# Kernel tuning notes

Hardware: AMD Instinct MI355X
Metric: run time of the kernel (lower is better)

The kernel has to match this reference:

```python
import jax, jax.numpy as jnp
import numpy as np

N, E, C, NEF, OUT, NUM_ANGLE = 20000, 160000, 32, 1, 128, 7
F = 2 * C + NEF  # edge_fdim = 65


def setup_inputs() -> dict:
    rng = np.random.default_rng(0)
    row = rng.integers(0, N, size=E).astype(np.int32)
    col = rng.integers(0, N, size=E).astype(np.int32)
    # Line-graph incidence pairs (a, b): edge a = (i,j) feeds edge b = (j,k), i.e. col[a] == row[b].
    sort_idx = np.argsort(row, kind='stable')
    row_sorted = row[sort_idx]
    starts = np.searchsorted(row_sorted, col, 'left')
    ends = np.searchsorted(row_sorted, col, 'right')
    counts = ends - starts
    total = int(counts.sum())
    line_src = np.repeat(np.arange(E, dtype=np.int32), counts)
    base = np.repeat(starts, counts)
    within = np.arange(total, dtype=np.int64) - np.repeat(np.cumsum(counts) - counts, counts)
    line_dst = sort_idx[base + within].astype(np.int32)

    key = jax.random.key(0)
    k = jax.random.split(key, 5)
    return {
        'x': jax.random.normal(k[0], (N, C), jnp.float32),
        'edge_attr': jax.random.normal(k[1], (E, NEF), jnp.float32),
        'pos': jax.random.normal(k[2], (N, 3), jnp.float32),
        'W_msg': jax.random.normal(k[3], (OUT, NUM_ANGLE * 2 * F), jnp.float32) * 0.02,
        'b_msg': jax.random.normal(k[4], (OUT,), jnp.float32) * 0.01,
        'edge_index': jnp.asarray(np.stack([row, col]), jnp.int32),
        'line_src': jnp.asarray(line_src),
        'line_dst': jnp.asarray(line_dst),
    }


def reference(x, edge_attr, pos, W_msg, b_msg, edge_index, line_src, line_dst):
    row, col = edge_index[0], edge_index[1]
    num_node = x.shape[0]
    num_edge = row.shape[0]

    # edge_f = [x_row | x_col | edge_attr]  -> [E, F]
    edge_f = jnp.concatenate([x[row], x[col], edge_attr], axis=1)

    # Line graph: edge a=(i,j) feeds edge b=(j,k). Angle at shared node j.
    j = col[line_src]
    u = pos[row[line_src]] - pos[j]  # j -> i
    v = pos[col[line_dst]] - pos[j]  # j -> k
    cos = jnp.sum(u * v, axis=-1) / (
        jnp.linalg.norm(u, axis=-1) * jnp.linalg.norm(v, axis=-1) + 1e-8)
    ang = jnp.arccos(jnp.clip(cos, -1.0 + 1e-7, 1.0 - 1e-7))  # [0, pi]
    abin = jnp.clip((ang / jnp.pi * NUM_ANGLE).astype(jnp.int32), 0, NUM_ANGLE - 1)

    # Per target edge, accumulate neighbor-edge features into (angle bin, in/out slot).
    seg_in = line_dst.astype(jnp.int32) * (NUM_ANGLE * 2) + abin * 2      # incoming a -> b
    seg_out = line_src.astype(jnp.int32) * (NUM_ANGLE * 2) + abin * 2 + 1  # outgoing b seen from a
    vals = jnp.concatenate([edge_f[line_src], edge_f[line_dst]], axis=0)  # [2L, F]
    segs = jnp.concatenate([seg_in, seg_out], axis=0)
    msg = jax.ops.segment_sum(vals, segs, num_segments=num_edge * NUM_ANGLE * 2)
    msg = msg.reshape(num_edge, NUM_ANGLE * 2 * F)  # [E, 910]

    # output = self.message(message)  (Linear with bias)
    edge_hidden = msg @ W_msg.T + b_msg  # [E, OUT]

    # scatter_add into destination nodes (edge_index[1])
    update = jax.ops.segment_sum(edge_hidden, col, num_segments=num_node)  # [N, OUT]
    return update
```

## Files before the change

### kernel.cpp

```cpp
#include <hip/hip_runtime.h>
#include <stdint.h>

#define N_NODES 20000
#define E_EDGES 160000
#define C_DIM 32
#define OUT_DIM 128
#define K_REAL 910
#define KPH 480
#define DEG_CAP 64
#define SEG 1024
#define NSEG 20
#define MT_A (E_EDGES/256)
#define NROWS_B 20224
#define MT_B (NROWS_B/256)

typedef __attribute__((ext_vector_type(4))) float f32x4;
typedef __attribute__((ext_vector_type(8))) short short8;

__device__ __forceinline__ float bf2f(unsigned short u){
  union { unsigned int i; float f; } v; v.i = ((unsigned int)u) << 16; return v.f;
}
__device__ __forceinline__ unsigned short f2bf(float f){
  union { float f; unsigned int i; } v; v.f = f;
  unsigned int i = v.i;
  unsigned int r = (i + 0x7FFFu + ((i >> 16) & 1u)) >> 16;
  return (unsigned short)r;
}
__device__ __forceinline__ float ldv(const void* p, size_t i, int isbf){
  return isbf ? bf2f(((const unsigned short*)p)[i]) : ((const float*)p)[i];
}
__device__ __forceinline__ int clampi(int v, int hi){
  return ((unsigned)v < (unsigned)hi) ? v : 0;
}

__global__ void k_sniff(const void* xraw, int* flag){
  const unsigned short* xu = (const unsigned short*)xraw;
  __shared__ int s_bad;
  int tid = threadIdx.x;
  if (tid == 0) s_bad = 0;
  __syncthreads();
  float v = bf2f(xu[tid * 2499]);
  if (!(fabsf(v) < 100.0f)) s_bad = 1;
  __syncthreads();
  if (tid == 0) flag[0] = s_bad ? 0 : 1;
}

__global__ void k_zero(int* p, int n){
  int i = blockIdx.x*blockDim.x + threadIdx.x;
  if (i < n) p[i] = 0;
}

__global__ void k_build(const void* __restrict__ pos,
                        const int* __restrict__ row, const int* __restrict__ col,
                        float* __restrict__ vecn, int* __restrict__ cnt,
                        const int* __restrict__ flg)
{
  int e = blockIdx.x*blockDim.x + threadIdx.x;
  if (e >= E_EDGES) return;
  int isbf = flg[0];
  int r = clampi(row[e], N_NODES), c = clampi(col[e], N_NODES);
  float vx = ldv(pos, (size_t)c*3+0, isbf) - ldv(pos, (size_t)r*3+0, isbf);
  float vy = ldv(pos, (size_t)c*3+1, isbf) - ldv(pos, (size_t)r*3+1, isbf);
  float vz = ldv(pos, (size_t)c*3+2, isbf) - ldv(pos, (size_t)r*3+2, isbf);
  float nn = sqrtf(vx*vx + vy*vy + vz*vz);
  f32x4 vv; vv[0]=vx; vv[1]=vy; vv[2]=vz; vv[3]=nn;
  *(f32x4*)(vecn + (size_t)e*4) = vv;
  atomicAdd(cnt + r, 1);
  atomicAdd(cnt + N_NODES + c, 1);
}

__global__ void k_scan1(const int* __restrict__ cnt, int* __restrict__ start2,
                        int* __restrict__ segsum){
  __shared__ int buf[SEG];
  int b = blockIdx.x, arr = b / NSEG, seg = b - arr*NSEG;
  const int* cntp = cnt + (size_t)arr*N_NODES;
  int* startp = start2 + (size_t)arr*(N_NODES+1);
  int tid = threadIdx.x;
  int i = seg*SEG + tid;
  int v = (i < N_NODES) ? cntp[i] : 0;
  buf[tid] = v;
  __syncthreads();
  for (int off = 1; off < SEG; off <<= 1){
    int t = (tid >= off) ? buf[tid-off] : 0;
    __syncthreads();
    buf[tid] += t;
    __syncthreads();
  }
  if (i < N_NODES) startp[i] = buf[tid] - v;
  if (tid == SEG-1) segsum[b] = buf[tid];
}
__global__ void k_scan2(int* segsum){
  int tid = threadIdx.x;
  if (tid < 2){
    int run = 0;
    for (int s = 0; s < NSEG; ++s){
      int v = segsum[tid*NSEG+s]; segsum[tid*NSEG+s] = run; run += v;
    }
  }
}
__global__ void k_scan3(int* __restrict__ start2, int* __restrict__ fill2,
                        const int* __restrict__ segsum){
  int b = blockIdx.x, arr = b / NSEG, seg = b - arr*NSEG;
  int* startp = start2 + (size_t)arr*(N_NODES+1);
  int* fillp  = fill2  + (size_t)arr*N_NODES;
  int tid = threadIdx.x;
  int i = seg*SEG + tid;
  int add = segsum[b];
  if (i < N_NODES){ int s = startp[i] + add; startp[i] = s; fillp[i] = s; }
  if (b == 0 && tid == 0){
    start2[N_NODES] = E_EDGES;
    start2[(N_NODES+1) + N_NODES] = E_EDGES;
  }
}

__global__ void k_scatter(const int* __restrict__ row, const int* __restrict__ col,
                          int* fill2, int* list_row, int* list_col,
                          int* pos_col, int* node_of_pos)
{
  int e = blockIdx.x*blockDim.x + threadIdx.x;
  if (e >= E_EDGES) return;
  int r = clampi(row[e], N_NODES), c = clampi(col[e], N_NODES);
  int p = atomicAdd(fill2 + r, 1);
  if ((unsigned)p < E_EDGES) list_row[p] = e;
  int q = atomicAdd(fill2 + N_NODES + c, 1);
  if ((unsigned)q < E_EDGES){ list_col[q] = e; node_of_pos[q] = c; }
  pos_col[e] = clampi(q, E_EDGES);
}

__global__ void k_packw(const void* __restrict__ W, unsigned short* __restrict__ Wp,
                        const int* __restrict__ flg){
  int isbf = flg[0];
  int i = blockIdx.x*blockDim.x + threadIdx.x;
  if (i >= 2*OUT_DIM*KPH) return;
  int half = i / (OUT_DIM*KPH);
  int rem = i - half*OUT_DIM*KPH;
  int o = rem / KPH, kp = rem - o*KPH;
  float v = 0.f;
  if (kp < 455){
    int t = kp/65, f = kp - t*65;
    v = ldv(W, (size_t)o*K_REAL + (2*t + half)*65 + f, isbf);
  }
  Wp[i] = f2bf(v);
}

__global__ __launch_bounds__(256)
void k_msg_node(const void* __restrict__ x, const void* __restrict__ eattr,
                const float* __restrict__ vecn,
                const int* __restrict__ row, const int* __restrict__ col,
                const int* __restrict__ start2,
                const int* __restrict__ list_row, const int* __restrict__ list_col,
                const int* __restrict__ pos_col,
                unsigned short* __restrict__ msg,
                const int* __restrict__ flg, int half)
{
  __shared__ int posT[DEG_CAP];
  __shared__ int othS[DEG_CAP];
  __shared__ float vS[DEG_CAP][4], vT[DEG_CAP][4];
  __shared__ float eS[DEG_CAP];
  __shared__ unsigned short fS[DEG_CAP][64];
  __shared__ float e64[DEG_CAP][8];
  __shared__ unsigned char bins[DEG_CAP][DEG_CAP];

  const float cb1 = 0.9009688679f, cb2 = 0.6234898019f, cb3 = 0.2225209340f;
  const int* start_row = start2;
  const int* start_col = start2 + (N_NODES+1);
  int j = blockIdx.x;
  int tid = threadIdx.x, wv = tid >> 6, lane = tid & 63;
  int clo = start_col[j], chi = start_col[j+1];
  int rlo = start_row[j], rhi = start_row[j+1];
  if (clo < 0) clo = 0; if (chi > E_EDGES) chi = E_EDGES; if (chi < clo) chi = clo;
  if (rlo < 0) rlo = 0; if (rhi > E_EDGES) rhi = E_EDGES; if (rhi < rlo) rhi = rlo;
  int nI = chi - clo, nO = rhi - rlo;
  int nS = half ? nO : nI;
  int nT = half ? nI : nO;
  int slo = half ? rlo : clo;
  int tlo = half ? clo : rlo;
  const int* slist = half ? list_row : list_col;
  const int* tlist = half ? list_col : list_row;
  if (nT == 0) return;
  int isbf = flg[0];

  if (nS <= DEG_CAP && nT <= DEG_CAP){
    int nS4 = (nS + 3) & ~3;
    if (tid < nS){
      int s = clampi(slist[slo+tid], E_EDGES);
      othS[tid] = clampi(half ? col[s] : row[s], N_NODES);
      eS[tid] = ldv(eattr, s, isbf);
      vS[tid][0]=vecn[s*4+0]; vS[tid][1]=vecn[s*4+1];
      vS[tid][2]=vecn[s*4+2]; vS[tid][3]=vecn[s*4+3];
    }
    if (tid < nT){
      int t = clampi(tlist[tlo+tid], E_EDGES);
      posT[tid] = clampi(pos_col[t], E_EDGES);
      vT[tid][0]=vecn[t*4+0]; vT[tid][1]=vecn[t*4+1];
      vT[tid][2]=vecn[t*4+2]; vT[tid][3]=vecn[t*4+3];
    }
    for (int i = tid; i < DEG_CAP*8; i += 256) ((float*)e64)[i] = 0.f;
    { uint4 z = {0,0,0,0};
      ((uint4*)bins)[tid] = z; }
    __syncthreads();
    for (int cidx = tid; cidx < nS*64; cidx += 256){
      int si = cidx >> 6, f = cidx & 63;
      int lo_node = half ? j : othS[si];
      int hi_node = half ? othS[si] : j;
      int src = (f < 32) ? (lo_node*C_DIM + f) : (hi_node*C_DIM + f - 32);
      fS[si][f] = f2bf(ldv(x, (size_t)src, isbf));
    }
    for (int i = tid; i < (nS4 - nS)*64; i += 256)
      fS[nS + (i >> 6)][i & 63] = 0;
    for (int p = tid; p < nS*64; p += 256){
      int si = p >> 6, ti = p & 63;
      if (ti < nT){
        float dot = -(vS[si][0]*vT[ti][0] + vS[si][1]*vT[ti][1] + vS[si][2]*vT[ti][2]);
        float cv = dot / (vS[si][3]*vT[ti][3] + 1e-8f);
        int t = (cv<=cb1)+(cv<=cb2)+(cv<=cb3)+(cv<=-cb3)+(cv<=-cb2)+(cv<=-cb1);
        bins[ti][si] = (unsigned char)t;
        atomicAdd(&e64[ti][t], eS[si]);
      }
    }
    __syncthreads();
    for (int ti = wv; ti < nT; ti += 4){
      float S0=0,S1=0,S2=0,S3=0,S4=0,S5=0,S6=0;
      const unsigned* brow = (const unsigned*)bins[ti];
      for (int s4 = 0; s4 < nS4; s4 += 4){
        unsigned bb = (unsigned)__builtin_amdgcn_readfirstlane((int)brow[s4 >> 2]);
        #pragma unroll
        for (int u = 0; u < 4; ++u){
          int t = (bb >> (8*u)) & 7;
          float val = bf2f(fS[s4 + u][lane]);
          switch(t){
            case 0: S0+=val; break; case 1: S1+=val; break; case 2: S2+=val; break;
            case 3: S3+=val; break; case 4: S4+=val; break; case 5: S5+=val; break;
            default: S6+=val; break;
          }
        }
      }
      unsigned short* mrow = msg + (size_t)posT[ti]*KPH;
      mrow[0*65+lane]=f2bf(S0); mrow[1*65+lane]=f2bf(S1); mrow[2*65+lane]=f2bf(S2);
      mrow[3*65+lane]=f2bf(S3); mrow[4*65+lane]=f2bf(S4); mrow[5*65+lane]=f2bf(S5);
      mrow[6*65+lane]=f2bf(S6);
      if (lane < 7)  mrow[lane*65+64] = f2bf(e64[ti][lane]);
      if (lane < 25) mrow[455+lane] = 0;
    }
  } else {
    for (int ti = wv; ti < nT; ti += 4){
      int te = clampi(tlist[tlo+ti], E_EDGES);
      float tx=vecn[te*4+0], ty=vecn[te*4+1], tz=vecn[te*4+2], tn=vecn[te*4+3];
      float S0=0,S1=0,S2=0,S3=0,S4=0,S5=0,S6=0,S64v=0;
      for (int si = 0; si < nS; ++si){
        int se = clampi(slist[slo+si], E_EDGES);
        float dot = -(vecn[se*4+0]*tx + vecn[se*4+1]*ty + vecn[se*4+2]*tz);
        float cv = dot / (vecn[se*4+3]*tn + 1e-8f);
        int tv = (cv<=cb1)+(cv<=cb2)+(cv<=cb3)+(cv<=-cb3)+(cv<=-cb2)+(cv<=-cb1);
        int t = __builtin_amdgcn_readfirstlane(tv);
        int oth = clampi(half ? col[se] : row[se], N_NODES);
        int lo_node = half ? j : oth;
        int hi_node = half ? oth : j;
        float val = (lane < 32) ? ldv(x, (size_t)lo_node*C_DIM+lane, isbf)
                                : ldv(x, (size_t)hi_node*C_DIM+lane-32, isbf);
        switch(t){
          case 0: S0+=val; break; case 1: S1+=val; break; case 2: S2+=val; break;
          case 3: S3+=val; break; case 4: S4+=val; break; case 5: S5+=val; break;
          default: S6+=val; break;
        }
        S64v += (lane == t) ? ldv(eattr, se, isbf) : 0.f;
      }
      unsigned short* mrow = msg + (size_t)clampi(pos_col[te], E_EDGES)*KPH;
      mrow[0*65+lane]=f2bf(S0); mrow[1*65+lane]=f2bf(S1); mrow[2*65+lane]=f2bf(S2);
      mrow[3*65+lane]=f2bf(S3); mrow[4*65+lane]=f2bf(S4); mrow[5*65+lane]=f2bf(S5);
      mrow[6*65+lane]=f2bf(S6);
      if (lane < 7)  mrow[lane*65+64] = f2bf(S64v);
      if (lane < 25) mrow[455+lane] = 0;
    }
  }
}

__global__ __launch_bounds__(256)
void k_msg1(const void* __restrict__ x, const void* __restrict__ eattr,
            const float* __restrict__ vecn,
            const int* __restrict__ row, const int* __restrict__ col,
            const int* __restrict__ start2,
            const int* __restrict__ list_row, const int* __restrict__ list_col,
            unsigned short* __restrict__ msgN,
            const int* __restrict__ flg)
{
  const float cb1 = 0.9009688679f, cb2 = 0.6234898019f, cb3 = 0.2225209340f;
  const int* start_row = start2;
  const int* start_col = start2 + (N_NODES+1);
  int wv = threadIdx.x >> 6, lane = threadIdx.x & 63;
  int j = blockIdx.x*4 + wv;
  if (j >= N_NODES) return;
  int isbf = flg[0];
  unsigned short* mrow = msgN + (size_t)j*KPH;

  int clo = start_col[j], chi = start_col[j+1];
  int rlo = start_row[j], rhi = start_row[j+1];
  if (clo < 0) clo = 0; if (chi > E_EDGES) chi = E_EDGES; if (chi < clo) chi = clo;
  if (rlo < 0) rlo = 0; if (rhi > E_EDGES) rhi = E_EDGES; if (rhi < rlo) rhi = rlo;
  int nS = chi - clo, nT = rhi - rlo;

  if (nT == 0 || nS == 0){
    for (int i = lane; i < KPH; i += 64) mrow[i] = 0;
    return;
  }

  float xjv = ldv(x, (size_t)j*C_DIM + (lane & 31), isbf);

  int svalid = lane < nS;
  int se = svalid ? clampi(list_col[clo + lane], E_EDGES) : 0;
  f32x4 vs = *(const f32x4*)(vecn + (size_t)se*4);
  int multi = (nS > 64);

  float m0=0,m1=0,m2=0,m3=0,m4=0,m5=0,m6=0;
  float me0=0,me1=0,me2=0,me3=0,me4=0,me5=0,me6=0;

  for (int ti = 0; ti < nT; ++ti){
    int te = __builtin_amdgcn_readfirstlane(clampi(list_row[rlo+ti], E_EDGES));
    f32x4 vt = *(const f32x4*)(vecn + (size_t)te*4);
    int oT = clampi(col[te], N_NODES);
    float eTv = ldv(eattr, te, isbf);
    int c0=0,c1=0,c2=0,c3=0,c4=0,c5=0,c6=0;
    if (!multi){
      float dot = -(vs[0]*vt[0] + vs[1]*vt[1] + vs[2]*vt[2]);
      float cv = dot / (vs[3]*vt[3] + 1e-8f);
      int t = (cv<=cb1)+(cv<=cb2)+(cv<=cb3)+(cv<=-cb3)+(cv<=-cb2)+(cv<=-cb1);
      if (!svalid) t = 7;
      c0 = __popcll(__ballot(t==0)); c1 = __popcll(__ballot(t==1));
      c2 = __popcll(__ballot(t==2)); c3 = __popcll(__ballot(t==3));
      c4 = __popcll(__ballot(t==4)); c5 = __popcll(__ballot(t==5));
      c6 = __popcll(__ballot(t==6));
    } else {
      for (int base = 0; base < nS; base += 64){
        int vvalid = (base + lane) < nS;
        int s2 = vvalid ? clampi(list_col[clo + base + lane], E_EDGES) : 0;
        f32x4 v2 = *(const f32x4*)(vecn + (size_t)s2*4);
        float dot = -(v2[0]*vt[0] + v2[1]*vt[1] + v2[2]*vt[2]);
        float cv = dot / (v2[3]*vt[3] + 1e-8f);
        int t = (cv<=cb1)+(cv<=cb2)+(cv<=cb3)+(cv<=-cb3)+(cv<=-cb2)+(cv<=-cb1);
        if (!vvalid) t = 7;
        c0 += __popcll(__ballot(t==0)); c1 += __popcll(__ballot(t==1));
        c2 += __popcll(__ballot(t==2)); c3 += __popcll(__ballot(t==3));
        c4 += __popcll(__ballot(t==4)); c5 += __popcll(__ballot(t==5));
        c6 += __popcll(__ballot(t==6));
      }
    }
    float valT = (lane < 32) ? xjv : ldv(x, (size_t)oT*C_DIM + lane - 32, isbf);
    m0 += (float)c0*valT; m1 += (float)c1*valT; m2 += (float)c2*valT;
    m3 += (float)c3*valT; m4 += (float)c4*valT; m5 += (float)c5*valT;
    m6 += (float)c6*valT;
    me0 += (float)c0*eTv; me1 += (float)c1*eTv; me2 += (float)c2*eTv;
    me3 += (float)c3*eTv; me4 += (float)c4*eTv; me5 += (float)c5*eTv;
    me6 += (float)c6*eTv;
  }

  mrow[0*65+lane]=f2bf(m0); mrow[1*65+lane]=f2bf(m1); mrow[2*65+lane]=f2bf(m2);
  mrow[3*65+lane]=f2bf(m3); mrow[4*65+lane]=f2bf(m4); mrow[5*65+lane]=f2bf(m5);
  mrow[6*65+lane]=f2bf(m6);
  if (lane < 7){
    float me = (lane==0)?me0:(lane==1)?me1:(lane==2)?me2:(lane==3)?me3
             : (lane==4)?me4:(lane==5)?me5:me6;
    mrow[lane*65+64] = f2bf(me);
  }
  if (lane < 25) mrow[455+lane] = 0;
}

__global__ __launch_bounds__(256)
void k_gemm(const unsigned short* __restrict__ A,
            const unsigned short* __restrict__ Wp,
            const void* __restrict__ bias,
            const int* __restrict__ flg,
            const int* __restrict__ node_of_pos,
            float* __restrict__ out_acc, int addbias, int ident, int mtiles)
{
  __shared__ union {
    unsigned short Bs[64*512];
    float seg[256][66];
  } sh;
  __shared__ int nids[256];

  int tid = threadIdx.x;
  int w = tid >> 6, lane = tid & 63;
  int lrow = lane & 15, q = lane >> 4;

  int lin = blockIdx.x;
  const int FULLG = (mtiles & ~7) * 2;
  int mt, ch;
  if (lin < FULLG){
    mt = (lin >> 4)*8 + (lin & 7);
    ch = (lin >> 3) & 1;
  } else {
    int r2 = lin - FULLG;
    mt = (mtiles & ~7) + (r2 >> 1);
    ch = r2 & 1;
  }
  int m0 = mt * 256;

  nids[tid] = ident ? ((m0 + tid < N_NODES) ? m0 + tid : N_NODES-1)
                    : clampi(node_of_pos[m0 + tid], N_NODES);

  const unsigned short* abase = A + (size_t)(m0 + w*64 + lrow)*KPH + q*8;
  short8 apf[3][4];
  #pragma unroll
  for (int d = 0; d < 3; ++d)
    #pragma unroll
    for (int rf = 0; rf < 4; ++rf)
      apf[d][rf] = *(const short8*)(abase + (size_t)rf*16*KPH + d*32);

  #pragma unroll
  for (int i = 0; i < 15; ++i){
    int idx = tid + i*256;
    int rr = idx / 60, cc = idx - rr*60;
    const uint4* gq = (const uint4*)(Wp + (size_t)(ch*64 + rr)*KPH + cc*8);
    *(uint4*)(sh.Bs + rr*512 + ((cc ^ (rr & 7))*8)) = *gq;
  }
  __syncthreads();

  f32x4 acc[4][4];
  #pragma unroll
  for (int rf = 0; rf < 4; ++rf)
    #pragma unroll
    for (int nf = 0; nf < 4; ++nf) acc[rf][nf] = (f32x4)0.f;

  #pragma unroll
  for (int k0i = 0; k0i < 15; ++k0i){
    int cur = k0i % 3;
    int c = k0i*4 + q;
    #pragma unroll
    for (int nf = 0; nf < 4; ++nf){
      int rb = nf*16 + lrow;
      short8 bfr = *(const short8*)(sh.Bs + rb*512 + ((c ^ (rb & 7))*8));
      #pragma unroll
      for (int rf = 0; rf < 4; ++rf)
        acc[rf][nf] = __builtin_amdgcn_mfma_f32_16x16x32_bf16(apf[cur][rf], bfr, acc[rf][nf], 0, 0, 0);
    }
    if (k0i + 3 < 15){
      #pragma unroll
      for (int rf = 0; rf < 4; ++rf)
        apf[cur][rf] = *(const short8*)(abase + (size_t)rf*16*KPH + (k0i+3)*32);
    }
  }

  int isbf = flg[0];
  float bvs[4];
  #pragma unroll
  for (int nf = 0; nf < 4; ++nf)
    bvs[nf] = addbias ? ldv(bias, ch*64 + nf*16 + lrow, isbf) : 0.f;

  __syncthreads();
  #pragma unroll
  for (int rf = 0; rf < 4; ++rf)
    #pragma unroll
    for (int r = 0; r < 4; ++r){
      int m = w*64 + rf*16 + q*4 + r;
      #pragma unroll
      for (int nf = 0; nf < 4; ++nf)
        sh.seg[m][nf*16 + lrow] = acc[rf][nf][r] + bvs[nf];
    }
  __syncthreads();
  {
    int o = tid & 63, g = tid >> 6;
    int base = g*64;
    float s = 0.f;
    int curn = nids[base];
    for (int r = 0; r < 64; ++r){
      int m = base + r;
      int nid = nids[m];
      if (nid != curn){
        atomicAdd(out_acc + (size_t)curn*OUT_DIM + ch*64 + o, s);
        s = 0.f; curn = nid;
      }
      s += sh.seg[m][o];
    }
    atomicAdd(out_acc + (size_t)curn*OUT_DIM + ch*64 + o, s);
  }
}

__global__ void k_out(const float* __restrict__ acc, void* __restrict__ outp,
                      const int* __restrict__ flg){
  int i = blockIdx.x*blockDim.x + threadIdx.x;
  if (i >= N_NODES*OUT_DIM) return;
  if (flg[0]) ((unsigned short*)outp)[i] = f2bf(acc[i]);
  else        ((float*)outp)[i] = acc[i];
}

extern "C" void kernel_launch(void* const* d_in, const int* in_sizes, int n_in,
                              void* d_out, int out_size, void* d_ws, size_t ws_size,
                              hipStream_t stream)
{
  const void* x     = d_in[0];
  const void* eattr = d_in[1];
  const void* pos   = d_in[2];
  const void* W     = d_in[3];
  const void* bmsg  = d_in[4];
  const int* eidx = (const int*)d_in[5];
  const int* row = eidx;
  const int* col = eidx + E_EDGES;

  char* ws = (char*)d_ws;
  size_t off = 0;
  auto alloc = [&](size_t b){ size_t o = off; off += (b + 255) & ~(size_t)255; return o; };

  int* dflag        = (int*)(ws + alloc(256));
  float* vecn       = (float*)(ws + alloc((size_t)E_EDGES*16));
  int* cnt          = (int*)(ws + alloc((size_t)2*N_NODES*4));
  int* start2       = (int*)(ws + alloc((size_t)2*(N_NODES+1)*4));
  int* fill2        = (int*)(ws + alloc((size_t)2*N_NODES*4));
  int* segsum       = (int*)(ws + alloc((size_t)2*NSEG*4));
  int* list_row     = (int*)(ws + alloc((size_t)E_EDGES*4));
  int* list_col     = (int*)(ws + alloc((size_t)E_EDGES*4));
  int* pos_col      = (int*)(ws + alloc((size_t)E_EDGES*4));
  int* node_of_pos  = (int*)(ws + alloc((size_t)E_EDGES*4));
  unsigned short* Wp = (unsigned short*)(ws + alloc((size_t)2*OUT_DIM*KPH*2));
  float* out_acc    = (float*)(ws + alloc((size_t)N_NODES*OUT_DIM*4));
  unsigned short* msgN = (unsigned short*)(ws + alloc((size_t)NROWS_B*KPH*2));
  unsigned short* msg  = (unsigned short*)(ws + alloc((size_t)E_EDGES*KPH*2));
  (void)off;

  unsigned short* Wp_in  = Wp;
  unsigned short* Wp_out = Wp + (size_t)OUT_DIM*KPH;

  k_sniff<<<1, 256, 0, stream>>>(x, dflag);
  k_zero<<<(2*N_NODES+255)/256, 256, 0, stream>>>(cnt, 2*N_NODES);
  k_zero<<<(N_NODES*OUT_DIM+255)/256, 256, 0, stream>>>((int*)out_acc, N_NODES*OUT_DIM);
  {
    int padw = (NROWS_B - N_NODES)*KPH/2;
    k_zero<<<(padw+255)/256, 256, 0, stream>>>((int*)(msgN + (size_t)N_NODES*KPH), padw);
  }
  k_build<<<(E_EDGES+255)/256, 256, 0, stream>>>(pos, row, col, vecn, cnt, dflag);
  k_scan1<<<2*NSEG, SEG, 0, stream>>>(cnt, start2, segsum);
  k_scan2<<<1, 64, 0, stream>>>(segsum);
  k_scan3<<<2*NSEG, SEG, 0, stream>>>(start2, fill2, segsum);
  k_scatter<<<(E_EDGES+255)/256, 256, 0, stream>>>(row, col, fill2,
                                                   list_row, list_col, pos_col, node_of_pos);
  k_packw<<<(2*OUT_DIM*KPH+255)/256, 256, 0, stream>>>(W, Wp, dflag);

  k_msg_node<<<N_NODES, 256, 0, stream>>>(x, eattr, vecn, row, col, start2,
                                          list_row, list_col, pos_col, msg, dflag, 0);
  k_msg1<<<(N_NODES+3)/4, 256, 0, stream>>>(x, eattr, vecn, row, col, start2,
                                            list_row, list_col, msgN, dflag);
  k_gemm<<<dim3(2*MT_A), 256, 0, stream>>>(msg, Wp_in, bmsg, dflag,
                                           node_of_pos, out_acc, 1, 0, MT_A);
  k_gemm<<<dim3(2*MT_B), 256, 0, stream>>>(msgN, Wp_out, bmsg, dflag,
                                           node_of_pos, out_acc, 0, 1, MT_B);

  k_out<<<(N_NODES*OUT_DIM+255)/256, 256, 0, stream>>>(out_acc, d_out, dflag);
}
```

Baseline: 334.4 us.

## Aggregate incoming-edge messages per node before GEMM instead of per edge

Instead of writing a 480-wide bf16 message row per edge and running a 160k-row GEMM, the incoming-message kernel now atomically accumulates partial sums into a per-destination-node fp32 buffer H. It also records per-edge angle-bin counts, which let the node-constant part be rebuilt per node. The weights are repacked to match the new column layout, both GEMMs are merged into one launch over node rows, and the bias is applied as count times bias in the output kernel. This removes the large per-edge message traffic and most of the GEMM work, in exchange for many float atomics on H and extra zeroing passes.

```diff
diff --git a/kernel.cpp b/kernel.cpp
--- a/kernel.cpp
+++ b/kernel.cpp
@@ -7,10 +7,10 @@
 #define OUT_DIM 128
 #define K_REAL 910
 #define KPH 480
+#define HSTR 240
 #define DEG_CAP 64
 #define SEG 1024
 #define NSEG 20
-#define MT_A (E_EDGES/256)
 #define NROWS_B 20224
 #define MT_B (NROWS_B/256)
 
@@ -115,7 +115,7 @@
 
 __global__ void k_scatter(const int* __restrict__ row, const int* __restrict__ col,
                           int* fill2, int* list_row, int* list_col,
-                          int* pos_col, int* node_of_pos)
+                          int* pos_col, int* row_of_pos)
 {
   int e = blockIdx.x*blockDim.x + threadIdx.x;
   if (e >= E_EDGES) return;
@@ -123,7 +123,7 @@
   int p = atomicAdd(fill2 + r, 1);
   if ((unsigned)p < E_EDGES) list_row[p] = e;
   int q = atomicAdd(fill2 + N_NODES + c, 1);
-  if ((unsigned)q < E_EDGES){ list_col[q] = e; node_of_pos[q] = c; }
+  if ((unsigned)q < E_EDGES){ list_col[q] = e; row_of_pos[q] = r; }
   pos_col[e] = clampi(q, E_EDGES);
 }
 
@@ -137,8 +137,14 @@
   int o = rem / KPH, kp = rem - o*KPH;
   float v = 0.f;
   if (kp < 455){
-    int t = kp/65, f = kp - t*65;
-    v = ldv(W, (size_t)o*K_REAL + (2*t + half)*65 + f, isbf);
+    int src;
+    if (half == 0){
+      if (kp < 231){ int t = kp/33, f = kp - t*33; src = 2*t*65 + ((f < 32) ? f : 64); }
+      else         { int c = kp - 231; int t = c >> 5, f = c & 31; src = 2*t*65 + 32 + f; }
+    } else {
+      int t = kp/65, f = kp - t*65; src = (2*t + 1)*65 + f;
+    }
+    v = ldv(W, (size_t)o*K_REAL + src, isbf);
   }
   Wp[i] = f2bf(v);
 }
@@ -150,11 +156,12 @@
                 const int* __restrict__ start2,
                 const int* __restrict__ list_row, const int* __restrict__ list_col,
                 const int* __restrict__ pos_col,
-                unsigned short* __restrict__ msg,
-                const int* __restrict__ flg, int half)
+                float* __restrict__ H, uint2* __restrict__ cntb,
+                const int* __restrict__ flg)
 {
   __shared__ int posT[DEG_CAP];
   __shared__ int othS[DEG_CAP];
+  __shared__ int othT[DEG_CAP];
   __shared__ float vS[DEG_CAP][4], vT[DEG_CAP][4];
   __shared__ float eS[DEG_CAP];
   __shared__ unsigned short fS[DEG_CAP][64];
@@ -170,28 +177,23 @@
   int rlo = start_row[j], rhi = start_row[j+1];
   if (clo < 0) clo = 0; if (chi > E_EDGES) chi = E_EDGES; if (chi < clo) chi = clo;
   if (rlo < 0) rlo = 0; if (rhi > E_EDGES) rhi = E_EDGES; if (rhi < rlo) rhi = rlo;
-  int nI = chi - clo, nO = rhi - rlo;
-  int nS = half ? nO : nI;
-  int nT = half ? nI : nO;
-  int slo = half ? rlo : clo;
-  int tlo = half ? clo : rlo;
-  const int* slist = half ? list_row : list_col;
-  const int* tlist = half ? list_col : list_row;
+  int nS = chi - clo, nT = rhi - rlo;
   if (nT == 0) return;
   int isbf = flg[0];
 
   if (nS <= DEG_CAP && nT <= DEG_CAP){
     int nS4 = (nS + 3) & ~3;
     if (tid < nS){
-      int s = clampi(slist[slo+tid], E_EDGES);
-      othS[tid] = clampi(half ? col[s] : row[s], N_NODES);
+      int s = clampi(list_col[clo+tid], E_EDGES);
+      othS[tid] = clampi(row[s], N_NODES);
       eS[tid] = ldv(eattr, s, isbf);
       vS[tid][0]=vecn[s*4+0]; vS[tid][1]=vecn[s*4+1];
       vS[tid][2]=vecn[s*4+2]; vS[tid][3]=vecn[s*4+3];
     }
     if (tid < nT){
-      int t = clampi(tlist[tlo+tid], E_EDGES);
+      int t = clampi(list_row[rlo+tid], E_EDGES);
       posT[tid] = clampi(pos_col[t], E_EDGES);
+      othT[tid] = clampi(col[t], N_NODES);
       vT[tid][0]=vecn[t*4+0]; vT[tid][1]=vecn[t*4+1];
       vT[tid][2]=vecn[t*4+2]; vT[tid][3]=vecn[t*4+3];
     }
@@ -201,9 +203,7 @@
     __syncthreads();
     for (int cidx = tid; cidx < nS*64; cidx += 256){
       int si = cidx >> 6, f = cidx & 63;
-      int lo_node = half ? j : othS[si];
-      int hi_node = half ? othS[si] : j;
-      int src = (f < 32) ? (lo_node*C_DIM + f) : (hi_node*C_DIM + f - 32);
+      int src = (f < 32) ? (othS[si]*C_DIM + f) : (j*C_DIM + f - 32);
       fS[si][f] = f2bf(ldv(x, (size_t)src, isbf));
     }
     for (int i = tid; i < (nS4 - nS)*64; i += 256)
@@ -235,124 +235,119 @@
           }
         }
       }
-      unsigned short* mrow = msg + (size_t)posT[ti]*KPH;
-      mrow[0*65+lane]=f2bf(S0); mrow[1*65+lane]=f2bf(S1); mrow[2*65+lane]=f2bf(S2);
-      mrow[3*65+lane]=f2bf(S3); mrow[4*65+lane]=f2bf(S4); mrow[5*65+lane]=f2bf(S5);
-      mrow[6*65+lane]=f2bf(S6);
-      if (lane < 7)  mrow[lane*65+64] = f2bf(e64[ti][lane]);
-      if (lane < 25) mrow[455+lane] = 0;
+      float* Hrow = H + (size_t)othT[ti]*HSTR;
+      if (lane < 32){
+        atomicAdd(Hrow + 0*33 + lane, S0);
+        atomicAdd(Hrow + 1*33 + lane, S1);
+        atomicAdd(Hrow + 2*33 + lane, S2);
+        atomicAdd(Hrow + 3*33 + lane, S3);
+        atomicAdd(Hrow + 4*33 + lane, S4);
+        atomicAdd(Hrow + 5*33 + lane, S5);
+        atomicAdd(Hrow + 6*33 + lane, S6);
+      }
+      if (lane < 7) atomicAdd(Hrow + lane*33 + 32, e64[ti][lane]);
+      int myb = (lane < nS) ? (int)bins[ti][lane] : 7;
+      unsigned n0 = (unsigned)__popcll(__ballot(myb==0));
+      unsigned n1 = (unsigned)__popcll(__ballot(myb==1));
+      unsigned n2 = (unsigned)__popcll(__ballot(myb==2));
+      unsigned n3 = (unsigned)__popcll(__ballot(myb==3));
+      unsigned n4 = (unsigned)__popcll(__ballot(myb==4));
+      unsigned n5 = (unsigned)__popcll(__ballot(myb==5));
+      unsigned n6 = (unsigned)__popcll(__ballot(myb==6));
+      if (lane == 0){
+        uint2 cw;
+        cw.x = n0 | (n1<<8) | (n2<<16) | (n3<<24);
+        cw.y = n4 | (n5<<8) | (n6<<16);
+        cntb[posT[ti]] = cw;
+      }
     }
   } else {
     for (int ti = wv; ti < nT; ti += 4){
-      int te = clampi(tlist[tlo+ti], E_EDGES);
+      int te = clampi(list_row[rlo+ti], E_EDGES);
       float tx=vecn[te*4+0], ty=vecn[te*4+1], tz=vecn[te*4+2], tn=vecn[te*4+3];
+      int nd = clampi(col[te], N_NODES);
       float S0=0,S1=0,S2=0,S3=0,S4=0,S5=0,S6=0,S64v=0;
+      int n0=0,n1=0,n2=0,n3=0,n4=0,n5=0,n6=0;
       for (int si = 0; si < nS; ++si){
-        int se = clampi(slist[slo+si], E_EDGES);
+        int se = clampi(list_col[clo+si], E_EDGES);
         float dot = -(vecn[se*4+0]*tx + vecn[se*4+1]*ty + vecn[se*4+2]*tz);
         float cv = dot / (vecn[se*4+3]*tn + 1e-8f);
         int tv = (cv<=cb1)+(cv<=cb2)+(cv<=cb3)+(cv<=-cb3)+(cv<=-cb2)+(cv<=-cb1);
         int t = __builtin_amdgcn_readfirstlane(tv);
-        int oth = clampi(half ? col[se] : row[se], N_NODES);
-        int lo_node = half ? j : oth;
-        int hi_node = half ? oth : j;
-        float val = (lane < 32) ? ldv(x, (size_t)lo_node*C_DIM+lane, isbf)
-                                : ldv(x, (size_t)hi_node*C_DIM+lane-32, isbf);
+        int oth = clampi(row[se], N_NODES);
+        float val = (lane < 32) ? ldv(x, (size_t)oth*C_DIM+lane, isbf)
+                                : ldv(x, (size_t)j*C_DIM+lane-32, isbf);
         switch(t){
-          case 0: S0+=val; break; case 1: S1+=val; break; case 2: S2+=val; break;
-          case 3: S3+=val; break; case 4: S4+=val; break; case 5: S5+=val; break;
-          default: S6+=val; break;
+          case 0: S0+=val; n0++; break; case 1: S1+=val; n1++; break;
+          case 2: S2+=val; n2++; break; case 3: S3+=val; n3++; break;
+          case 4: S4+=val; n4++; break; case 5: S5+=val; n5++; break;
+          default: S6+=val; n6++; break;
         }
         S64v += (lane == t) ? ldv(eattr, se, isbf) : 0.f;
       }
-      unsigned short* mrow = msg + (size_t)clampi(pos_col[te], E_EDGES)*KPH;
-      mrow[0*65+lane]=f2bf(S0); mrow[1*65+lane]=f2bf(S1); mrow[2*65+lane]=f2bf(S2);
-      mrow[3*65+lane]=f2bf(S3); mrow[4*65+lane]=f2bf(S4); mrow[5*65+lane]=f2bf(S5);
-      mrow[6*65+lane]=f2bf(S6);
-      if (lane < 7)  mrow[lane*65+64] = f2bf(S64v);
-      if (lane < 25) mrow[455+lane] = 0;
+      float* Hrow = H + (size_t)nd*HSTR;
+      if (lane < 32){
+        atomicAdd(Hrow + 0*33 + lane, S0);
+        atomicAdd(Hrow + 1*33 + lane, S1);
+        atomicAdd(Hrow + 2*33 + lane, S2);
+        atomicAdd(Hrow + 3*33 + lane, S3);
+        atomicAdd(Hrow + 4*33 + lane, S4);
+        atomicAdd(Hrow + 5*33 + lane, S5);
+        atomicAdd(Hrow + 6*33 + lane, S6);
+      }
+      if (lane < 7) atomicAdd(Hrow + lane*33 + 32, S64v);
+      if (lane == 0){
+        uint2 cw;
+        cw.x = (unsigned)min(n0,255) | ((unsigned)min(n1,255)<<8)
+             | ((unsigned)min(n2,255)<<16) | ((unsigned)min(n3,255)<<24);
+        cw.y = (unsigned)min(n4,255) | ((unsigned)min(n5,255)<<8)
+             | ((unsigned)min(n6,255)<<16);
+        cntb[clampi(pos_col[te], E_EDGES)] = cw;
+      }
     }
   }
 }
 
 __global__ __launch_bounds__(256)
 void k_msg1(const void* __restrict__ x, const void* __restrict__ eattr,
-            const float* __restrict__ vecn,
-            const int* __restrict__ row, const int* __restrict__ col,
+            const int* __restrict__ col,
             const int* __restrict__ start2,
-            const int* __restrict__ list_row, const int* __restrict__ list_col,
+            const int* __restrict__ list_row, const int* __restrict__ pos_col,
+            const uint2* __restrict__ cntb,
             unsigned short* __restrict__ msgN,
             const int* __restrict__ flg)
 {
-  const float cb1 = 0.9009688679f, cb2 = 0.6234898019f, cb3 = 0.2225209340f;
   const int* start_row = start2;
-  const int* start_col = start2 + (N_NODES+1);
   int wv = threadIdx.x >> 6, lane = threadIdx.x & 63;
   int j = blockIdx.x*4 + wv;
   if (j >= N_NODES) return;
   int isbf = flg[0];
   unsigned short* mrow = msgN + (size_t)j*KPH;
-
-  int clo = start_col[j], chi = start_col[j+1];
   int rlo = start_row[j], rhi = start_row[j+1];
-  if (clo < 0) clo = 0; if (chi > E_EDGES) chi = E_EDGES; if (chi < clo) chi = clo;
   if (rlo < 0) rlo = 0; if (rhi > E_EDGES) rhi = E_EDGES; if (rhi < rlo) rhi = rlo;
-  int nS = chi - clo, nT = rhi - rlo;
-
-  if (nT == 0 || nS == 0){
+  int nT = rhi - rlo;
+  if (nT == 0){
     for (int i = lane; i < KPH; i += 64) mrow[i] = 0;
     return;
   }
-
-  float xjv = ldv(x, (size_t)j*C_DIM + (lane & 31), isbf);
-
-  int svalid = lane < nS;
-  int se = svalid ? clampi(list_col[clo + lane], E_EDGES) : 0;
-  f32x4 vs = *(const f32x4*)(vecn + (size_t)se*4);
-  int multi = (nS > 64);
-
+  float xj = ldv(x, (size_t)j*C_DIM + (lane & 31), isbf);
   float m0=0,m1=0,m2=0,m3=0,m4=0,m5=0,m6=0;
   float me0=0,me1=0,me2=0,me3=0,me4=0,me5=0,me6=0;
-
   for (int ti = 0; ti < nT; ++ti){
     int te = __builtin_amdgcn_readfirstlane(clampi(list_row[rlo+ti], E_EDGES));
-    f32x4 vt = *(const f32x4*)(vecn + (size_t)te*4);
+    int p  = __builtin_amdgcn_readfirstlane(clampi(pos_col[te], E_EDGES));
+    uint2 cw = cntb[p];
+    unsigned cx = (unsigned)__builtin_amdgcn_readfirstlane((int)cw.x);
+    unsigned cy = (unsigned)__builtin_amdgcn_readfirstlane((int)cw.y);
     int oT = clampi(col[te], N_NODES);
-    float eTv = ldv(eattr, te, isbf);
-    int c0=0,c1=0,c2=0,c3=0,c4=0,c5=0,c6=0;
-    if (!multi){
-      float dot = -(vs[0]*vt[0] + vs[1]*vt[1] + vs[2]*vt[2]);
-      float cv = dot / (vs[3]*vt[3] + 1e-8f);
-      int t = (cv<=cb1)+(cv<=cb2)+(cv<=cb3)+(cv<=-cb3)+(cv<=-cb2)+(cv<=-cb1);
-      if (!svalid) t = 7;
-      c0 = __popcll(__ballot(t==0)); c1 = __popcll(__ballot(t==1));
-      c2 = __popcll(__ballot(t==2)); c3 = __popcll(__ballot(t==3));
-      c4 = __popcll(__ballot(t==4)); c5 = __popcll(__ballot(t==5));
-      c6 = __popcll(__ballot(t==6));
-    } else {
-      for (int base = 0; base < nS; base += 64){
-        int vvalid = (base + lane) < nS;
-        int s2 = vvalid ? clampi(list_col[clo + base + lane], E_EDGES) : 0;
-        f32x4 v2 = *(const f32x4*)(vecn + (size_t)s2*4);
-        float dot = -(v2[0]*vt[0] + v2[1]*vt[1] + v2[2]*vt[2]);
-        float cv = dot / (v2[3]*vt[3] + 1e-8f);
-        int t = (cv<=cb1)+(cv<=cb2)+(cv<=cb3)+(cv<=-cb3)+(cv<=-cb2)+(cv<=-cb1);
-        if (!vvalid) t = 7;
-        c0 += __popcll(__ballot(t==0)); c1 += __popcll(__ballot(t==1));
-        c2 += __popcll(__ballot(t==2)); c3 += __popcll(__ballot(t==3));
-        c4 += __popcll(__ballot(t==4)); c5 += __popcll(__ballot(t==5));
-        c6 += __popcll(__ballot(t==6));
-      }
-    }
-    float valT = (lane < 32) ? xjv : ldv(x, (size_t)oT*C_DIM + lane - 32, isbf);
-    m0 += (float)c0*valT; m1 += (float)c1*valT; m2 += (float)c2*valT;
-    m3 += (float)c3*valT; m4 += (float)c4*valT; m5 += (float)c5*valT;
-    m6 += (float)c6*valT;
-    me0 += (float)c0*eTv; me1 += (float)c1*eTv; me2 += (float)c2*eTv;
-    me3 += (float)c3*eTv; me4 += (float)c4*eTv; me5 += (float)c5*eTv;
-    me6 += (float)c6*eTv;
-  }
-
+    float eb = ldv(eattr, te, isbf);
+    float val = (lane < 32) ? xj : ldv(x, (size_t)oT*C_DIM + lane - 32, isbf);
+    float n0=(float)(cx&255u), n1=(float)((cx>>8)&255u), n2=(float)((cx>>16)&255u),
+          n3=(float)(cx>>24), n4=(float)(cy&255u), n5=(float)((cy>>8)&255u),
+          n6=(float)((cy>>16)&255u);
+    m0+=n0*val; m1+=n1*val; m2+=n2*val; m3+=n3*val; m4+=n4*val; m5+=n5*val; m6+=n6*val;
+    me0+=n0*eb; me1+=n1*eb; me2+=n2*eb; me3+=n3*eb; me4+=n4*eb; me5+=n5*eb; me6+=n6*eb;
+  }
   mrow[0*65+lane]=f2bf(m0); mrow[1*65+lane]=f2bf(m1); mrow[2*65+lane]=f2bf(m2);
   mrow[3*65+lane]=f2bf(m3); mrow[4*65+lane]=f2bf(m4); mrow[5*65+lane]=f2bf(m5);
   mrow[6*65+lane]=f2bf(m6);
@@ -365,38 +360,73 @@
 }
 
 __global__ __launch_bounds__(256)
-void k_gemm(const unsigned short* __restrict__ A,
-            const unsigned short* __restrict__ Wp,
-            const void* __restrict__ bias,
-            const int* __restrict__ flg,
-            const int* __restrict__ node_of_pos,
-            float* __restrict__ out_acc, int addbias, int ident, int mtiles)
+void k_gh(const void* __restrict__ x, const float* __restrict__ H,
+          const int* __restrict__ start2,
+          const int* __restrict__ row_of_pos, const uint2* __restrict__ cntb,
+          unsigned short* __restrict__ rowA, const int* __restrict__ flg)
+{
+  const int* start_col = start2 + (N_NODES+1);
+  int wv = threadIdx.x >> 6, lane = threadIdx.x & 63;
+  int j = blockIdx.x*4 + wv;
+  if (j >= N_NODES) return;
+  int isbf = flg[0];
+  unsigned short* ar = rowA + (size_t)j*KPH;
+  int clo = start_col[j], chi = start_col[j+1];
+  if (clo < 0) clo = 0; if (chi > E_EDGES) chi = E_EDGES; if (chi < clo) chi = clo;
+  int f = lane & 31, g = lane >> 5;
+  float m0=0, m1=0, m2=0, m3=0;
+  for (int p = clo; p < chi; ++p){
+    uint2 cw = cntb[p];
+    unsigned cx = (unsigned)__builtin_amdgcn_readfirstlane((int)cw.x);
+    unsigned cy = (unsigned)__builtin_amdgcn_readfirstlane((int)cw.y);
+    int jj = __builtin_amdgcn_readfirstlane(clampi(row_of_pos[p], N_NODES));
+    float xv = ldv(x, (size_t)jj*C_DIM + f, isbf);
+    float a0, a1, a2, a3;
+    if (g == 0){ a0=(float)(cx&255u); a1=(float)((cx>>16)&255u);
+                 a2=(float)(cy&255u); a3=(float)((cy>>16)&255u); }
+    else       { a0=(float)((cx>>8)&255u); a1=(float)(cx>>24);
+                 a2=(float)((cy>>8)&255u); a3=0.f; }
+    m0 += a0*xv; m1 += a1*xv; m2 += a2*xv; m3 += a3*xv;
+  }
+  const float* Hrow = H + (size_t)j*HSTR;
+  for (int c = lane; c < 231; c += 64) ar[c] = f2bf(Hrow[c]);
+  ar[231 + (g+0)*32 + f] = f2bf(m0);
+  ar[231 + (g+2)*32 + f] = f2bf(m1);
+  ar[231 + (g+4)*32 + f] = f2bf(m2);
+  if (g + 6 < 7) ar[231 + (g+6)*32 + f] = f2bf(m3);
+  if (lane < 25) ar[455 + lane] = 0;
+}
+
+__global__ __launch_bounds__(256)
+void k_gemmN(const unsigned short* __restrict__ A1, const unsigned short* __restrict__ W1,
+             const unsigned short* __restrict__ A2, const unsigned short* __restrict__ W2,
+             float* __restrict__ out_acc)
 {
   __shared__ union {
     unsigned short Bs[64*512];
     float seg[256][66];
   } sh;
-  __shared__ int nids[256];
 
   int tid = threadIdx.x;
   int w = tid >> 6, lane = tid & 63;
   int lrow = lane & 15, q = lane >> 4;
 
-  int lin = blockIdx.x;
-  const int FULLG = (mtiles & ~7) * 2;
+  int which = (blockIdx.x >= 2*MT_B) ? 1 : 0;
+  int lin = blockIdx.x - which*2*MT_B;
+  const unsigned short* A  = which ? A2 : A1;
+  const unsigned short* Wp = which ? W2 : W1;
+
+  const int FULLG = (MT_B & ~7) * 2;
   int mt, ch;
   if (lin < FULLG){
     mt = (lin >> 4)*8 + (lin & 7);
     ch = (lin >> 3) & 1;
   } else {
     int r2 = lin - FULLG;
-    mt = (mtiles & ~7) + (r2 >> 1);
+    mt = (MT_B & ~7) + (r2 >> 1);
     ch = r2 & 1;
   }
   int m0 = mt * 256;
-
-  nids[tid] = ident ? ((m0 + tid < N_NODES) ? m0 + tid : N_NODES-1)
-                    : clampi(node_of_pos[m0 + tid], N_NODES);
 
   const unsigned short* abase = A + (size_t)(m0 + w*64 + lrow)*KPH + q*8;
   short8 apf[3][4];
@@ -440,12 +470,6 @@
     }
   }
 
-  int isbf = flg[0];
-  float bvs[4];
-  #pragma unroll
-  for (int nf = 0; nf < 4; ++nf)
-    bvs[nf] = addbias ? ldv(bias, ch*64 + nf*16 + lrow, isbf) : 0.f;
-
   __syncthreads();
   #pragma unroll
   for (int rf = 0; rf < 4; ++rf)
@@ -454,33 +478,30 @@
       int m = w*64 + rf*16 + q*4 + r;
       #pragma unroll
       for (int nf = 0; nf < 4; ++nf)
-        sh.seg[m][nf*16 + lrow] = acc[rf][nf][r] + bvs[nf];
+        sh.seg[m][nf*16 + lrow] = acc[rf][nf][r];
     }
   __syncthreads();
   {
     int o = tid & 63, g = tid >> 6;
     int base = g*64;
-    float s = 0.f;
-    int curn = nids[base];
     for (int r = 0; r < 64; ++r){
-      int m = base + r;
-      int nid = nids[m];
-      if (nid != curn){
-        atomicAdd(out_acc + (size_t)curn*OUT_DIM + ch*64 + o, s);
-        s = 0.f; curn = nid;
-      }
-      s += sh.seg[m][o];
-    }
-    atomicAdd(out_acc + (size_t)curn*OUT_DIM + ch*64 + o, s);
-  }
-}
-
-__global__ void k_out(const float* __restrict__ acc, void* __restrict__ outp,
+      int nid = m0 + base + r;
+      if (nid >= N_NODES) nid = N_NODES - 1;
+      atomicAdd(out_acc + (size_t)nid*OUT_DIM + ch*64 + o, sh.seg[base + r][o]);
+    }
+  }
+}
+
+__global__ void k_out(const float* __restrict__ acc, const int* __restrict__ cnt,
+                      const void* __restrict__ bias, void* __restrict__ outp,
                       const int* __restrict__ flg){
   int i = blockIdx.x*blockDim.x + threadIdx.x;
   if (i >= N_NODES*OUT_DIM) return;
-  if (flg[0]) ((unsigned short*)outp)[i] = f2bf(acc[i]);
-  else        ((float*)outp)[i] = acc[i];
+  int n = i >> 7, o = i & 127;
+  int isbf = flg[0];
+  float v = acc[i] + (float)cnt[N_NODES + n] * ldv(bias, o, isbf);
+  if (isbf) ((unsigned short*)outp)[i] = f2bf(v);
+  else      ((float*)outp)[i] = v;
 }
 
 extern "C" void kernel_launch(void* const* d_in, const int* in_sizes, int n_in,
@@ -509,39 +530,42 @@
   int* list_row     = (int*)(ws + alloc((size_t)E_EDGES*4));
   int* list_col     = (int*)(ws + alloc((size_t)E_EDGES*4));
   int* pos_col      = (int*)(ws + alloc((size_t)E_EDGES*4));
-  int* node_of_pos  = (int*)(ws + alloc((size_t)E_EDGES*4));
+  int* row_of_pos   = (int*)(ws + alloc((size_t)E_EDGES*4));
   unsigned short* Wp = (unsigned short*)(ws + alloc((size_t)2*OUT_DIM*KPH*2));
   float* out_acc    = (float*)(ws + alloc((size_t)N_NODES*OUT_DIM*4));
   unsigned short* msgN = (unsigned short*)(ws + alloc((size_t)NROWS_B*KPH*2));
-  unsigned short* msg  = (unsigned short*)(ws + alloc((size_t)E_EDGES*KPH*2));
+  unsigned short* rowA = (unsigned short*)(ws + alloc((size_t)NROWS_B*KPH*2));
+  float* H          = (float*)(ws + alloc((size_t)N_NODES*HSTR*4));
+  uint2* cntb       = (uint2*)(ws + alloc((size_t)E_EDGES*8));
   (void)off;
 
-  unsigned short* Wp_in  = Wp;
-  unsigned short* Wp_out = Wp + (size_t)OUT_DIM*KPH;
+  unsigned short* Wp0 = Wp;
+  unsigned short* Wp1 = Wp + (size_t)OUT_DIM*KPH;
 
   k_sniff<<<1, 256, 0, stream>>>(x, dflag);
   k_zero<<<(2*N_NODES+255)/256, 256, 0, stream>>>(cnt, 2*N_NODES);
   k_zero<<<(N_NODES*OUT_DIM+255)/256, 256, 0, stream>>>((int*)out_acc, N_NODES*OUT_DIM);
+  k_zero<<<((N_NODES*HSTR)+255)/256, 256, 0, stream>>>((int*)H, N_NODES*HSTR);
+  k_zero<<<(E_EDGES*2+255)/256, 256, 0, stream>>>((int*)cntb, E_EDGES*2);
   {
     int padw = (NROWS_B - N_NODES)*KPH/2;
     k_zero<<<(padw+255)/256, 256, 0, stream>>>((int*)(msgN + (size_t)N_NODES*KPH), padw);
+    k_zero<<<(padw+255)/256, 256, 0, stream>>>((int*)(rowA + (size_t)N_NODES*KPH), padw);
   }
   k_build<<<(E_EDGES+255)/256, 256, 0, stream>>>(pos, row, col, vecn, cnt, dflag);
   k_scan1<<<2*NSEG, SEG, 0, stream>>>(cnt, start2, segsum);
   k_scan2<<<1, 64, 0, stream>>>(segsum);
   k_scan3<<<2*NSEG, SEG, 0, stream>>>(start2, fill2, segsum);
   k_scatter<<<(E_EDGES+255)/256, 256, 0, stream>>>(row, col, fill2,
-                                                   list_row, list_col, pos_col, node_of_pos);
+                                                   list_row, list_col, pos_col, row_of_pos);
   k_packw<<<(2*OUT_DIM*KPH+255)/256, 256, 0, stream>>>(W, Wp, dflag);
 
   k_msg_node<<<N_NODES, 256, 0, stream>>>(x, eattr, vecn, row, col, start2,
-                                          list_row, list_col, pos_col, msg, dflag, 0);
-  k_msg1<<<(N_NODES+3)/4, 256, 0, stream>>>(x, eattr, vecn, row, col, start2,
-                                            list_row, list_col, msgN, dflag);
-  k_gemm<<<dim3(2*MT_A), 256, 0, stream>>>(msg, Wp_in, bmsg, dflag,
-                                           node_of_pos, out_acc, 1, 0, MT_A);
-  k_gemm<<<dim3(2*MT_B), 256, 0, stream>>>(msgN, Wp_out, bmsg, dflag,
-                                           node_of_pos, out_acc, 0, 1, MT_B);
-
-  k_out<<<(N_NODES*OUT_DIM+255)/256, 256, 0, stream>>>(out_acc, d_out, dflag);
-}
+                                          list_row, list_col, pos_col, H, cntb, dflag);
+  k_msg1<<<(N_NODES+3)/4, 256, 0, stream>>>(x, eattr, col, start2,
+                                            list_row, pos_col, cntb, msgN, dflag);
+  k_gh<<<(N_NODES+3)/4, 256, 0, stream>>>(x, H, start2, row_of_pos, cntb, rowA, dflag);
+  k_gemmN<<<dim3(4*MT_B), 256, 0, stream>>>(rowA, Wp0, msgN, Wp1, out_acc);
+
+  k_out<<<(N_NODES*OUT_DIM+255)/256, 256, 0, stream>>>(out_acc, cnt, bmsg, d_out, dflag);
+}
```

After: 489.2 us. 46.3% more time.
